# Optimization experiments

Measured on AMD Instinct MI355X. Metric: run time of the kernel, lower is better.

## Reference

```python
import jax, jax.numpy as jnp
import numpy as np

B, N, HIDDEN, IN_DIM = 4, 1024, 64, 6


def setup_inputs() -> dict:
    key = jax.random.key(0)
    ks = jax.random.split(key, 8)
    pos = jax.random.normal(ks[0], (B, N, 3), dtype=jnp.float32)
    vel = jax.random.normal(ks[1], (B, N, 3), dtype=jnp.float32)
    # edge MLP params (Linear stores W as [out,in] in torch; we use [in,out])
    s1 = 1.0 / np.sqrt(IN_DIM)
    s2 = 1.0 / np.sqrt(HIDDEN)
    W1 = jax.random.uniform(ks[2], (IN_DIM, HIDDEN), jnp.float32, -s1, s1)
    b1 = jax.random.uniform(ks[3], (HIDDEN,), jnp.float32, -s1, s1)
    W2 = jax.random.uniform(ks[4], (HIDDEN, HIDDEN), jnp.float32, -s2, s2)
    b2 = jax.random.uniform(ks[5], (HIDDEN,), jnp.float32, -s2, s2)
    W3 = jax.random.uniform(ks[6], (HIDDEN, 3), jnp.float32, -s2, s2)
    b3 = jax.random.uniform(ks[7], (3,), jnp.float32, -s2, s2)
    return {"pos": pos, "vel": vel, "W1": W1, "b1": b1, "W2": W2, "b2": b2, "W3": W3, "b3": b3}


def reference(pos, vel, W1, b1, W2, b2, W3, b3):
    # all-pairs differences: r_ij[b,i,j] = pos[b,j] - pos[b,i]   [B,N,N,3]
    r_ij = pos[:, None, :, :] - pos[:, :, None, :]
    v_ij = vel[:, None, :, :] - vel[:, :, None, :]
    edge_inputs = jnp.concatenate([r_ij, v_ij], axis=-1)  # [B,N,N,6]
    h = jax.nn.relu(jnp.einsum('bijk,kh->bijh', edge_inputs, W1) + b1)
    h = jax.nn.relu(jnp.einsum('bijh,hg->bijg', h, W2) + b2)
    f_ij = jnp.einsum('bijg,go->bijo', h, W3) + b3  # [B,N,N,3]
    # antisymmetrize over (i,j); diagonal becomes exactly 0
    f_sym = (f_ij - jnp.swapaxes(f_ij, 1, 2)) * 0.5
    acc = jnp.sum(f_sym, axis=2)  # [B,N,3]
    return acc
```

## Files before the change

### kernel.cpp

```cpp
#include <hip/hip_runtime.h>

#define NB   4
#define NPTS 1024
#define HID  64
#define TPB  64
#define UPB  2080

typedef float f32x4 __attribute__((ext_vector_type(4)));
typedef float f32x2 __attribute__((ext_vector_type(2)));
typedef short bf16x8 __attribute__((ext_vector_type(8)));
typedef unsigned int u32;
typedef unsigned short u16;

__device__ inline u16 f2bf(float x) {
    union { float f; unsigned u; } v; v.f = x;
    return (u16)((v.u + 0x7FFFu + ((v.u >> 16) & 1u)) >> 16);
}
__device__ inline u32 cvt_pk_bf16(float lo, float hi) {
    u32 r; asm("v_cvt_pk_bf16_f32 %0, %1, %2" : "=v"(r) : "v"(lo), "v"(hi)); return r;
}
__device__ inline u32 pk_relu2(u32 a) {
    u32 r; asm("v_pk_max_i16 %0, %1, 0" : "=v"(r) : "v"(a)); return r;
}

__global__ __launch_bounds__(256) void precompute(
    const float* __restrict__ pos, const float* __restrict__ vel,
    const float* __restrict__ W1, const float* __restrict__ W2,
    float* __restrict__ P, u16* __restrict__ W2T) {
    if (blockIdx.x == NB * NPTS / 4) {
        for (int e = threadIdx.x; e < HID * HID; e += 256) {
            const int ch = e >> 6, k = e & 63;
            W2T[e] = f2bf(W2[k * HID + ch]);
        }
        return;
    }
    const int t   = blockIdx.x * 256 + threadIdx.x;
    const int row = t >> 6;
    const int k   = t & 63;
    const float* pp = pos + row * 3;
    const float* vv = vel + row * 3;
    float acc = 0.f;
    #pragma unroll
    for (int c = 0; c < 3; ++c) acc = fmaf(pp[c], W1[c * HID + k], acc);
    #pragma unroll
    for (int c = 0; c < 3; ++c) acc = fmaf(vv[c], W1[(3 + c) * HID + k], acc);
    P[row * HID + k] = acc;
}

__device__ inline void emit_tile(const f32x4 Ht[4], float sgn, int rowbase,
                                 const float* __restrict__ W3,
                                 float* __restrict__ F, int c, int g) {
    #pragma unroll
    for (int r = 0; r < 4; ++r) {
        float f0 = 0.f, f1 = 0.f, f2 = 0.f;
        #pragma unroll
        for (int n = 0; n < 4; ++n) {
            const int ch = n * 16 + c;
            const float h = Ht[n][r];
            f0 = fmaf(h, W3[ch * 3 + 0], f0);
            f1 = fmaf(h, W3[ch * 3 + 1], f1);
            f2 = fmaf(h, W3[ch * 3 + 2], f2);
        }
        #pragma unroll
        for (int off = 1; off < 16; off <<= 1) {
            f0 += __shfl_xor(f0, off, 64);
            f1 += __shfl_xor(f1, off, 64);
            f2 += __shfl_xor(f2, off, 64);
        }
        if (c < 3) {
            const float v = (c == 0) ? f0 : ((c == 1) ? f1 : f2);
            atomicAdd(&F[(size_t)(rowbase + g * 4 + r) * 3 + c], sgn * v);
        }
    }
}

__global__ __launch_bounds__(128, 2) void inet_pair(
    const float* __restrict__ P,  const float* __restrict__ b1,
    const u16* __restrict__ W2T,  const float* __restrict__ b2,
    const float* __restrict__ W3, float* __restrict__ F) {
    const int tid  = threadIdx.x;
    const int lane = tid & 63;
    const int c    = lane & 15;
    const int g    = lane >> 4;

    const int unit = blockIdx.x * 2 + (tid >> 6);
    const int b    = unit / UPB;
    const int p    = unit - b * UPB;
    int I = (int)((129.0f - sqrtf((float)(16641 - 8 * p))) * 0.5f);
    while (I * (129 - I) / 2 > p) --I;
    while ((I + 1) * (128 - I) / 2 <= p) ++I;
    const int J = I + (p - I * (129 - I) / 2);
    const bool diag = (I == J);

    const float* Pb   = P + (size_t)b * NPTS * HID;
    const int    koff = g * 8;

    union V4 { f32x4 v; f32x2 p[2]; };

    bf16x8 Bf[8];
    #pragma unroll
    for (int kk = 0; kk < 2; ++kk)
        #pragma unroll
        for (int n = 0; n < 4; ++n)
            Bf[kk * 4 + n] = *(const bf16x8*)(W2T + (size_t)(n * 16 + c) * HID + kk * 32 + g * 8);

    f32x2 pj2[8];
    {
        const float* base = Pb + (size_t)(J * 16 + c) * HID + koff;
        V4 v0, v1, v2, v3;
        v0.v = *(const f32x4*)(base);
        v1.v = *(const f32x4*)(base + 4);
        v2.v = *(const f32x4*)(base + 32);
        v3.v = *(const f32x4*)(base + 36);
        pj2[0] = v0.p[0]; pj2[1] = v0.p[1]; pj2[2] = v1.p[0]; pj2[3] = v1.p[1];
        pj2[4] = v2.p[0]; pj2[5] = v2.p[1]; pj2[6] = v3.p[0]; pj2[7] = v3.p[1];
    }
    f32x2 bb2[8];
    {
        V4 v0, v1, v2, v3;
        v0.v = *(const f32x4*)(b1 + koff);
        v1.v = *(const f32x4*)(b1 + koff + 4);
        v2.v = *(const f32x4*)(b1 + koff + 32);
        v3.v = *(const f32x4*)(b1 + koff + 36);
        bb2[0] = v0.p[0]; bb2[1] = v0.p[1]; bb2[2] = v1.p[0]; bb2[3] = v1.p[1];
        bb2[4] = v2.p[0]; bb2[5] = v2.p[1]; bb2[6] = v3.p[0]; bb2[7] = v3.p[1];
    }
    float b2v[4];
    #pragma unroll
    for (int n = 0; n < 4; ++n) b2v[n] = b2[n * 16 + c];

    f32x4 Hi[4], Hj[4];
    #pragma unroll
    for (int n = 0; n < 4; ++n) {
        Hi[n] = (f32x4){0.f, 0.f, 0.f, 0.f};
        Hj[n] = (f32x4){0.f, 0.f, 0.f, 0.f};
    }

    const float* Pi0 = Pb + (size_t)(I * 16) * HID + koff;

    for (int i1 = 0; i1 < 4; ++i1) {
        const bool sel = (g == i1);
        #pragma unroll
        for (int i2 = 0; i2 < 4; ++i2) {
            const float* pib = Pi0 + (size_t)(i1 * 4 + i2) * HID;
            V4 w0, w1, w2, w3;
            w0.v = *(const f32x4*)(pib);
            w1.v = *(const f32x4*)(pib + 4);
            w2.v = *(const f32x4*)(pib + 32);
            w3.v = *(const f32x4*)(pib + 36);
            f32x2 pi2[8];
            pi2[0] = w0.p[0]; pi2[1] = w0.p[1]; pi2[2] = w1.p[0]; pi2[3] = w1.p[1];
            pi2[4] = w2.p[0]; pi2[5] = w2.p[1]; pi2[6] = w3.p[0]; pi2[7] = w3.p[1];

            union { bf16x8 v; u32 u[4]; } ap[2], am[2];
            #pragma unroll
            for (int kk = 0; kk < 2; ++kk)
                #pragma unroll
                for (int d = 0; d < 4; ++d) {
                    f32x2 u  = pi2[kk * 4 + d] - pj2[kk * 4 + d];
                    f32x2 tp = bb2[kk * 4 + d] - u;
                    f32x2 tm = bb2[kk * 4 + d] + u;
                    ap[kk].u[d] = pk_relu2(cvt_pk_bf16(tp.x, tp.y));
                    am[kk].u[d] = pk_relu2(cvt_pk_bf16(tm.x, tm.y));
                }

            #pragma unroll
            for (int n = 0; n < 4; ++n) {
                const f32x4 Ci = {b2v[n], b2v[n], b2v[n], b2v[n]};
                f32x4 Cp = __builtin_amdgcn_mfma_f32_16x16x32_bf16(ap[0].v, Bf[n],     Ci, 0, 0, 0);
                Cp       = __builtin_amdgcn_mfma_f32_16x16x32_bf16(ap[1].v, Bf[4 + n], Cp, 0, 0, 0);
                f32x4 Cm = __builtin_amdgcn_mfma_f32_16x16x32_bf16(am[0].v, Bf[n],     Ci, 0, 0, 0);
                Cm       = __builtin_amdgcn_mfma_f32_16x16x32_bf16(am[1].v, Bf[4 + n], Cm, 0, 0, 0);
                V4 dd;
                dd.p[0] = (f32x2){fmaxf(Cp[0], 0.f) - fmaxf(Cm[0], 0.f),
                                  fmaxf(Cp[1], 0.f) - fmaxf(Cm[1], 0.f)};
                dd.p[1] = (f32x2){fmaxf(Cp[2], 0.f) - fmaxf(Cm[2], 0.f),
                                  fmaxf(Cp[3], 0.f) - fmaxf(Cm[3], 0.f)};
                if (!diag) {
                    Hj[n][0] += dd.v[0]; Hj[n][1] += dd.v[1];
                    Hj[n][2] += dd.v[2]; Hj[n][3] += dd.v[3];
                }
                f32x2 q = dd.p[0] + dd.p[1];
                float s = q.x + q.y;
                s += __shfl_xor(s, 16, 64);
                s += __shfl_xor(s, 32, 64);
                Hi[n][i2] += sel ? s : 0.0f;
            }
        }
    }

    const int rowbase = b * NPTS;
    emit_tile(Hi, 0.5f, rowbase + I * 16, W3, F, c, g);
    if (!diag)
        emit_tile(Hj, -0.5f, rowbase + J * 16, W3, F, c, g);
}

extern "C" void kernel_launch(void* const* d_in, const int* in_sizes, int n_in,
                              void* d_out, int out_size, void* d_ws, size_t ws_size,
                              hipStream_t stream) {
    const float* pos = (const float*)d_in[0];
    const float* vel = (const float*)d_in[1];
    const float* W1  = (const float*)d_in[2];
    const float* b1  = (const float*)d_in[3];
    const float* W2  = (const float*)d_in[4];
    const float* b2  = (const float*)d_in[5];
    const float* W3  = (const float*)d_in[6];
    const float* b3  = (const float*)d_in[7];
    (void)b3;
    float* out = (float*)d_out;
    float* P   = (float*)d_ws;
    u16*   W2T = (u16*)((char*)d_ws + (size_t)NB * NPTS * HID * 4);

    hipMemsetAsync(out, 0, (size_t)out_size * sizeof(float), stream);
    precompute<<<dim3(NB * NPTS / 4 + 1), dim3(256), 0, stream>>>(pos, vel, W1, W2, P, W2T);
    inet_pair<<<dim3(NB * UPB / 2), dim3(128), 0, stream>>>(P, b1, W2T, b2, W3, out);
}
```

Measured before the change: 106.3 us.

## Process two j-tiles per wave to reuse i-tile loads and reductions

Each wave now handles one i-tile against a pair of adjacent j-tiles (2m, 2m+1), using a new triangular index mapping with 1056 units per batch instead of 2080 single pairs. The i-row loads, the cross-lane shuffle reduction for Hi, and the Hi atomic emission are shared across both j-tiles, which halves their per-pair cost. In exchange it holds more registers (two pj sets, two Hj accumulators), which may hurt occupancy under the 128x2 launch bound. Some waves also do half-idle work on edge units where the first j-tile is skipped.

```diff
diff --git a/kernel.cpp b/kernel.cpp
--- a/kernel.cpp
+++ b/kernel.cpp
@@ -3,8 +3,7 @@
 #define NB   4
 #define NPTS 1024
 #define HID  64
-#define TPB  64
-#define UPB  2080
+#define NU   1056
 
 typedef float f32x4 __attribute__((ext_vector_type(4)));
 typedef float f32x2 __attribute__((ext_vector_type(2)));
@@ -74,6 +73,44 @@
     }
 }
 
+__device__ inline void do_jt(const f32x2* __restrict__ pj2,
+                             const f32x2* __restrict__ bb2,
+                             const f32x2* __restrict__ pi2,
+                             const bf16x8* __restrict__ Bf,
+                             const float* __restrict__ b2v,
+                             bool accHj, f32x4* __restrict__ Hj,
+                             float* __restrict__ qout) {
+    union { bf16x8 v; u32 u[4]; } ap[2], am[2];
+    #pragma unroll
+    for (int kk = 0; kk < 2; ++kk)
+        #pragma unroll
+        for (int d = 0; d < 4; ++d) {
+            f32x2 u  = pi2[kk * 4 + d] - pj2[kk * 4 + d];
+            f32x2 tp = bb2[kk * 4 + d] - u;
+            f32x2 tm = bb2[kk * 4 + d] + u;
+            ap[kk].u[d] = pk_relu2(cvt_pk_bf16(tp.x, tp.y));
+            am[kk].u[d] = pk_relu2(cvt_pk_bf16(tm.x, tm.y));
+        }
+    #pragma unroll
+    for (int n = 0; n < 4; ++n) {
+        const f32x4 Ci = {b2v[n], b2v[n], b2v[n], b2v[n]};
+        f32x4 Cp = __builtin_amdgcn_mfma_f32_16x16x32_bf16(ap[0].v, Bf[n],     Ci, 0, 0, 0);
+        Cp       = __builtin_amdgcn_mfma_f32_16x16x32_bf16(ap[1].v, Bf[4 + n], Cp, 0, 0, 0);
+        f32x4 Cm = __builtin_amdgcn_mfma_f32_16x16x32_bf16(am[0].v, Bf[n],     Ci, 0, 0, 0);
+        Cm       = __builtin_amdgcn_mfma_f32_16x16x32_bf16(am[1].v, Bf[4 + n], Cm, 0, 0, 0);
+        f32x2 d01 = {fmaxf(Cp[0], 0.f) - fmaxf(Cm[0], 0.f),
+                     fmaxf(Cp[1], 0.f) - fmaxf(Cm[1], 0.f)};
+        f32x2 d23 = {fmaxf(Cp[2], 0.f) - fmaxf(Cm[2], 0.f),
+                     fmaxf(Cp[3], 0.f) - fmaxf(Cm[3], 0.f)};
+        if (accHj) {
+            Hj[n][0] += d01.x; Hj[n][1] += d01.y;
+            Hj[n][2] += d23.x; Hj[n][3] += d23.y;
+        }
+        f32x2 q = d01 + d23;
+        qout[n] = q.x + q.y;
+    }
+}
+
 __global__ __launch_bounds__(128, 2) void inet_pair(
     const float* __restrict__ P,  const float* __restrict__ b1,
     const u16* __restrict__ W2T,  const float* __restrict__ b2,
@@ -84,13 +121,16 @@
     const int g    = lane >> 4;
 
     const int unit = blockIdx.x * 2 + (tid >> 6);
-    const int b    = unit / UPB;
-    const int p    = unit - b * UPB;
-    int I = (int)((129.0f - sqrtf((float)(16641 - 8 * p))) * 0.5f);
-    while (I * (129 - I) / 2 > p) --I;
-    while ((I + 1) * (128 - I) / 2 <= p) ++I;
-    const int J = I + (p - I * (129 - I) / 2);
-    const bool diag = (I == J);
+    const int b    = unit / NU;
+    const int u    = unit - b * NU;
+    int m = (int)((sqrtf((float)(4 * u + 1)) - 1.0f) * 0.5f);
+    while (m * (m + 1) > u) --m;
+    while ((m + 1) * (m + 2) <= u) ++m;
+    const int I  = u - m * (m + 1);
+    const int J0 = 2 * m, J1 = 2 * m + 1;
+    const bool jt0act = (I != J1);
+    const bool diag0  = (I == J0);
+    const bool diag1  = (I == J1);
 
     const float* Pb   = P + (size_t)b * NPTS * HID;
     const int    koff = g * 8;
@@ -104,18 +144,7 @@
         for (int n = 0; n < 4; ++n)
             Bf[kk * 4 + n] = *(const bf16x8*)(W2T + (size_t)(n * 16 + c) * HID + kk * 32 + g * 8);
 
-    f32x2 pj2[8];
-    {
-        const float* base = Pb + (size_t)(J * 16 + c) * HID + koff;
-        V4 v0, v1, v2, v3;
-        v0.v = *(const f32x4*)(base);
-        v1.v = *(const f32x4*)(base + 4);
-        v2.v = *(const f32x4*)(base + 32);
-        v3.v = *(const f32x4*)(base + 36);
-        pj2[0] = v0.p[0]; pj2[1] = v0.p[1]; pj2[2] = v1.p[0]; pj2[3] = v1.p[1];
-        pj2[4] = v2.p[0]; pj2[5] = v2.p[1]; pj2[6] = v3.p[0]; pj2[7] = v3.p[1];
-    }
-    f32x2 bb2[8];
+    f32x2 bb2[8], pj0[8], pj1[8];
     {
         V4 v0, v1, v2, v3;
         v0.v = *(const f32x4*)(b1 + koff);
@@ -125,21 +154,42 @@
         bb2[0] = v0.p[0]; bb2[1] = v0.p[1]; bb2[2] = v1.p[0]; bb2[3] = v1.p[1];
         bb2[4] = v2.p[0]; bb2[5] = v2.p[1]; bb2[6] = v3.p[0]; bb2[7] = v3.p[1];
     }
+    {
+        const float* base = Pb + (size_t)(J0 * 16 + c) * HID + koff;
+        V4 v0, v1, v2, v3;
+        v0.v = *(const f32x4*)(base);
+        v1.v = *(const f32x4*)(base + 4);
+        v2.v = *(const f32x4*)(base + 32);
+        v3.v = *(const f32x4*)(base + 36);
+        pj0[0] = v0.p[0]; pj0[1] = v0.p[1]; pj0[2] = v1.p[0]; pj0[3] = v1.p[1];
+        pj0[4] = v2.p[0]; pj0[5] = v2.p[1]; pj0[6] = v3.p[0]; pj0[7] = v3.p[1];
+    }
+    {
+        const float* base = Pb + (size_t)(J1 * 16 + c) * HID + koff;
+        V4 v0, v1, v2, v3;
+        v0.v = *(const f32x4*)(base);
+        v1.v = *(const f32x4*)(base + 4);
+        v2.v = *(const f32x4*)(base + 32);
+        v3.v = *(const f32x4*)(base + 36);
+        pj1[0] = v0.p[0]; pj1[1] = v0.p[1]; pj1[2] = v1.p[0]; pj1[3] = v1.p[1];
+        pj1[4] = v2.p[0]; pj1[5] = v2.p[1]; pj1[6] = v3.p[0]; pj1[7] = v3.p[1];
+    }
     float b2v[4];
     #pragma unroll
     for (int n = 0; n < 4; ++n) b2v[n] = b2[n * 16 + c];
 
-    f32x4 Hi[4], Hj[4];
+    f32x4 Hi[4], Hj0[4], Hj1[4];
     #pragma unroll
     for (int n = 0; n < 4; ++n) {
-        Hi[n] = (f32x4){0.f, 0.f, 0.f, 0.f};
-        Hj[n] = (f32x4){0.f, 0.f, 0.f, 0.f};
+        Hi[n]  = (f32x4){0.f, 0.f, 0.f, 0.f};
+        Hj0[n] = (f32x4){0.f, 0.f, 0.f, 0.f};
+        Hj1[n] = (f32x4){0.f, 0.f, 0.f, 0.f};
     }
 
     const float* Pi0 = Pb + (size_t)(I * 16) * HID + koff;
 
     for (int i1 = 0; i1 < 4; ++i1) {
-        const bool sel = (g == i1);
+        const float selm = (g == i1) ? 1.0f : 0.0f;
         #pragma unroll
         for (int i2 = 0; i2 < 4; ++i2) {
             const float* pib = Pi0 + (size_t)(i1 * 4 + i2) * HID;
@@ -152,47 +202,30 @@
             pi2[0] = w0.p[0]; pi2[1] = w0.p[1]; pi2[2] = w1.p[0]; pi2[3] = w1.p[1];
             pi2[4] = w2.p[0]; pi2[5] = w2.p[1]; pi2[6] = w3.p[0]; pi2[7] = w3.p[1];
 
-            union { bf16x8 v; u32 u[4]; } ap[2], am[2];
-            #pragma unroll
-            for (int kk = 0; kk < 2; ++kk)
-                #pragma unroll
-                for (int d = 0; d < 4; ++d) {
-                    f32x2 u  = pi2[kk * 4 + d] - pj2[kk * 4 + d];
-                    f32x2 tp = bb2[kk * 4 + d] - u;
-                    f32x2 tm = bb2[kk * 4 + d] + u;
-                    ap[kk].u[d] = pk_relu2(cvt_pk_bf16(tp.x, tp.y));
-                    am[kk].u[d] = pk_relu2(cvt_pk_bf16(tm.x, tm.y));
-                }
+            float q0[4], q1[4];
+            if (jt0act) {
+                do_jt(pj0, bb2, pi2, Bf, b2v, !diag0, Hj0, q0);
+            } else {
+                q0[0] = q0[1] = q0[2] = q0[3] = 0.f;
+            }
+            do_jt(pj1, bb2, pi2, Bf, b2v, !diag1, Hj1, q1);
 
             #pragma unroll
             for (int n = 0; n < 4; ++n) {
-                const f32x4 Ci = {b2v[n], b2v[n], b2v[n], b2v[n]};
-                f32x4 Cp = __builtin_amdgcn_mfma_f32_16x16x32_bf16(ap[0].v, Bf[n],     Ci, 0, 0, 0);
-                Cp       = __builtin_amdgcn_mfma_f32_16x16x32_bf16(ap[1].v, Bf[4 + n], Cp, 0, 0, 0);
-                f32x4 Cm = __builtin_amdgcn_mfma_f32_16x16x32_bf16(am[0].v, Bf[n],     Ci, 0, 0, 0);
-                Cm       = __builtin_amdgcn_mfma_f32_16x16x32_bf16(am[1].v, Bf[4 + n], Cm, 0, 0, 0);
-                V4 dd;
-                dd.p[0] = (f32x2){fmaxf(Cp[0], 0.f) - fmaxf(Cm[0], 0.f),
-                                  fmaxf(Cp[1], 0.f) - fmaxf(Cm[1], 0.f)};
-                dd.p[1] = (f32x2){fmaxf(Cp[2], 0.f) - fmaxf(Cm[2], 0.f),
-                                  fmaxf(Cp[3], 0.f) - fmaxf(Cm[3], 0.f)};
-                if (!diag) {
-                    Hj[n][0] += dd.v[0]; Hj[n][1] += dd.v[1];
-                    Hj[n][2] += dd.v[2]; Hj[n][3] += dd.v[3];
-                }
-                f32x2 q = dd.p[0] + dd.p[1];
-                float s = q.x + q.y;
+                float s = q0[n] + q1[n];
                 s += __shfl_xor(s, 16, 64);
                 s += __shfl_xor(s, 32, 64);
-                Hi[n][i2] += sel ? s : 0.0f;
+                Hi[n][i2] = fmaf(selm, s, Hi[n][i2]);
             }
         }
     }
 
     const int rowbase = b * NPTS;
     emit_tile(Hi, 0.5f, rowbase + I * 16, W3, F, c, g);
-    if (!diag)
-        emit_tile(Hj, -0.5f, rowbase + J * 16, W3, F, c, g);
+    if (jt0act && !diag0)
+        emit_tile(Hj0, -0.5f, rowbase + J0 * 16, W3, F, c, g);
+    if (!diag1)
+        emit_tile(Hj1, -0.5f, rowbase + J1 * 16, W3, F, c, g);
 }
 
 extern "C" void kernel_launch(void* const* d_in, const int* in_sizes, int n_in,
@@ -213,5 +246,5 @@
 
     hipMemsetAsync(out, 0, (size_t)out_size * sizeof(float), stream);
     precompute<<<dim3(NB * NPTS / 4 + 1), dim3(256), 0, stream>>>(pos, vel, W1, W2, P, W2T);
-    inet_pair<<<dim3(NB * UPB / 2), dim3(128), 0, stream>>>(P, b1, W2T, b2, W3, out);
-}
+    inet_pair<<<dim3(NB * NU / 2), dim3(128), 0, stream>>>(P, b1, W2T, b2, W3, out);
+}
```

New measurement: 102.9 us. -3.2%, faster.
